# Kernel optimization log

Hardware: AMD Instinct MI355X
Metric: run time of the kernel (lower is better)

## Reference

```python
import jax, jax.numpy as jnp
import numpy as np

B, N, D = 8, 1024, 768
H = 12
HD = D // H


def setup_inputs() -> dict:
    key = jax.random.key(0)
    ks = jax.random.split(key, 9)
    s = 1.0 / np.sqrt(D)
    return {
        "x": jax.random.normal(ks[0], (B, N, D), dtype=jnp.float32),
        "Wq": jax.random.normal(ks[1], (D, D), dtype=jnp.float32) * s,
        "bq": jax.random.normal(ks[2], (D,), dtype=jnp.float32) * 0.02,
        "Wk": jax.random.normal(ks[3], (D, D), dtype=jnp.float32) * s,
        "bk": jax.random.normal(ks[4], (D,), dtype=jnp.float32) * 0.02,
        "Wv": jax.random.normal(ks[5], (D, D), dtype=jnp.float32) * s,
        "bv": jax.random.normal(ks[6], (D,), dtype=jnp.float32) * 0.02,
        "Wo": jax.random.normal(ks[7], (D, D), dtype=jnp.float32) * s,
        "bo": jax.random.normal(ks[8], (D,), dtype=jnp.float32) * 0.02,
    }


def _softmax_one(x):
    # quiet softmax: exp(x - max) / (1 + sum exp(x - max))
    x = x - jnp.max(x, axis=-1, keepdims=True)
    ex = jnp.exp(x)
    return ex / (1.0 + jnp.sum(ex, axis=-1, keepdims=True))


def reference(x, Wq, bq, Wk, bk, Wv, bv, Wo, bo):
    q = x @ Wq + bq  # [B,N,D]
    k = x @ Wk + bk
    v = x @ Wv + bv
    # split heads -> [B,H,N,HD]
    qs = q.reshape(B, N, H, HD).transpose(0, 2, 1, 3)
    ks = k.reshape(B, N, H, HD).transpose(0, 2, 1, 3)
    vs = v.reshape(B, N, H, HD).transpose(0, 2, 1, 3)
    scores = jnp.einsum("bhqd,bhkd->bhqk", qs, ks) / np.sqrt(HD)
    attn = _softmax_one(scores)  # quiet_attention=True
    ctx = jnp.einsum("bhqk,bhkd->bhqd", attn, vs)
    ctx = ctx.transpose(0, 2, 1, 3).reshape(B, N, D)
    return ctx @ Wo + bo
```

## Files before the change

### kernel.cpp

```cpp
#include <hip/hip_runtime.h>
#include <cstdint>

#define DEV __device__ __forceinline__

typedef __bf16 bf16x4 __attribute__((ext_vector_type(4)));
typedef __bf16 bf16x8 __attribute__((ext_vector_type(8)));
typedef float  floatx4 __attribute__((ext_vector_type(4)));
typedef float  floatx16 __attribute__((ext_vector_type(16)));
typedef unsigned uint4v __attribute__((ext_vector_type(4)));

constexpr int BB = 8, NSEQ = 1024, DMODEL = 768, NH = 12, HD = 64;
constexpr int MTOK = BB * NSEQ;
constexpr int NQKV = 3 * DMODEL;
constexpr float CS = 0.18033688011112042f;

DEV void async_copy16(void* lds, const void* g) {
    __builtin_amdgcn_global_load_lds(
        (__attribute__((address_space(1))) void*)(const_cast<void*>(g)),
        (__attribute__((address_space(3))) void*)lds,
        16, 0, 0);
}

DEV floatx4 mfma16x32(bf16x8 a, bf16x8 b, floatx4 c) {
    return __builtin_amdgcn_mfma_f32_16x16x32_bf16(a, b, c, 0, 0, 0);
}
DEV floatx16 mfma32x16(bf16x8 a, bf16x8 b, floatx16 c) {
    return __builtin_amdgcn_mfma_f32_32x32x16_bf16(a, b, c, 0, 0, 0);
}
DEV unsigned cvtpk(float a, float b) {
    unsigned r;
    asm("v_cvt_pk_bf16_f32 %0, %1, %2" : "=v"(r) : "v"(a), "v"(b));
    return r;
}
DEV void swap32(unsigned& x, unsigned& y) {
    asm("v_permlane32_swap_b32 %0, %1" : "+v"(x), "+v"(y));
}


__global__ __launch_bounds__(256) void k_prep(const float* __restrict__ x,
                                              __bf16* __restrict__ xb,
                                              const float* __restrict__ Wq,
                                              const float* __restrict__ Wk,
                                              const float* __restrict__ Wv,
                                              const float* __restrict__ Wo,
                                              __bf16* __restrict__ wtqkv,
                                              __bf16* __restrict__ wto,
                                              const float* __restrict__ bq,
                                              const float* __restrict__ bk,
                                              const float* __restrict__ bv,
                                              float* __restrict__ bqkv) {
    __shared__ float tile[32][33];
    int bid = blockIdx.x, t = threadIdx.x;
    if (bid < 6144) {
        int i = (bid * 256 + t) * 4;
        float4 v = *(const float4*)(x + i);
        bf16x4 o;
        o[0] = (__bf16)v.x; o[1] = (__bf16)v.y; o[2] = (__bf16)v.z; o[3] = (__bf16)v.w;
        *(bf16x4*)(xb + i) = o;
    } else if (bid < 8448) {
        int idx = bid - 6144;
        int z = idx / 576, rem = idx % 576;
        int k0 = (rem % 24) * 32, n0 = (rem / 24) * 32;
        const float* W = (z == 0) ? Wq : (z == 1) ? Wk : (z == 2) ? Wv : Wo;
        int tx = t & 31, ty = t >> 5;
#pragma unroll
        for (int p = 0; p < 4; p++)
            tile[ty + 8 * p][tx] = W[(size_t)(k0 + ty + 8 * p) * 768 + n0 + tx];
        __syncthreads();
        __bf16* out = (z < 3) ? (wtqkv + (size_t)z * 768 * 768) : wto;
#pragma unroll
        for (int p = 0; p < 4; p++)
            out[(size_t)(n0 + ty + 8 * p) * 768 + k0 + tx] = (__bf16)tile[tx][ty + 8 * p];
    } else {
        int i = (bid - 8448) * 256 + t;
        if (i < 768) bqkv[i] = bq[i];
        else if (i < 1536) bqkv[i] = bk[i - 768];
        else bqkv[i] = bv[i - 1536];
    }
}

__global__ __launch_bounds__(512) void k_qkv(const __bf16* __restrict__ A,
                                             const __bf16* __restrict__ Bt,
                                             const float* __restrict__ bias,
                                             __bf16* __restrict__ qfb,
                                             __bf16* __restrict__ kfb,
                                             __bf16* __restrict__ vfb) {
    constexpr int SLOT = 24576;
    __shared__ __align__(16) __bf16 lds[3 * SLOT];
    int t = threadIdx.x, lane = t & 63, w = t >> 6;
    int quad = lane >> 4, n16 = lane & 15;
    int wm = w >> 1, wn = w & 1;
    int m0 = blockIdx.x * 256, n0 = blockIdx.y * 128;
    floatx4 acc[4][4] = {};

    auto stage_part = [&](__bf16* slot, int k0, int p) {
        __bf16* As_ = slot;
        __bf16* Bs_ = slot + 16384;
#pragma unroll
        for (int i = 2 * p; i < 2 * p + 2; i++) {
            int off = t + i * 512;
            int row = off >> 3, pc = off & 7;
            int c = pc ^ (row & 7);
            async_copy16(&As_[row * 64 + pc * 8],
                         &A[(size_t)(m0 + row) * 768 + k0 + c * 8]);
        }
        {
            int off = t + p * 512;
            int row = off >> 3, pc = off & 7;
            int c = pc ^ (row & 7);
            async_copy16(&Bs_[row * 64 + pc * 8],
                         &Bt[(size_t)(n0 + row) * 768 + k0 + c * 8]);
        }
    };

    stage_part(lds, 0, 0);
    stage_part(lds, 0, 1);
    stage_part(lds + SLOT, 64, 0);
    stage_part(lds + SLOT, 64, 1);
    asm volatile("s_waitcnt vmcnt(6)\n\ts_barrier" ::: "memory");
    __builtin_amdgcn_sched_barrier(0);

#pragma unroll
    for (int kt = 0; kt < 12; kt++) {
        __bf16* As_ = lds + (kt % 3) * SLOT;
        __bf16* Bs_ = As_ + 16384;
        __bf16* pf = lds + ((kt + 2) % 3) * SLOT;
        int pk0 = (kt + 2) * 64;
        bool do_pf = (kt + 2 < 12);

#pragma unroll
        for (int kfi = 0; kfi < 2; kfi++) {
            if (do_pf) stage_part(pf, pk0, kfi);
            bf16x8 a[4], bfr[4];
#pragma unroll
            for (int rt = 0; rt < 4; rt++) {
                int row = wm * 64 + rt * 16 + n16;
                a[rt] = *(const bf16x8*)&As_[row * 64 + ((quad + 4 * kfi) ^ (row & 7)) * 8];
            }
#pragma unroll
            for (int ct = 0; ct < 4; ct++) {
                int row = wn * 64 + ct * 16 + n16;
                bfr[ct] = *(const bf16x8*)&Bs_[row * 64 + ((quad + 4 * kfi) ^ (row & 7)) * 8];
            }
            __builtin_amdgcn_s_setprio(1);
#pragma unroll
            for (int rt = 0; rt < 4; rt++)
#pragma unroll
                for (int ct = 0; ct < 4; ct++)
                    acc[rt][ct] = mfma16x32(a[rt], bfr[ct], acc[rt][ct]);
            __builtin_amdgcn_s_setprio(0);
        }

        if (kt < 11) {
            __builtin_amdgcn_sched_barrier(0);
            if (kt < 10) {
                asm volatile("s_waitcnt vmcnt(6)\n\ts_barrier" ::: "memory");
            } else {
                asm volatile("s_waitcnt vmcnt(0)\n\ts_barrier" ::: "memory");
            }
            __builtin_amdgcn_sched_barrier(0);
        }
    }

    if (n0 >= 1536) {
#pragma unroll
        for (int ct = 0; ct < 4; ct++) {
            int col = n0 + wn * 64 + ct * 16 + n16;
            float bs = bias[col];
            int cz = col - 1536;
            int hh = cz >> 6, hd = cz & 63;
            int mg = hd >> 5, l5v = hd & 31;
#pragma unroll
            for (int rt = 0; rt < 4; rt++) {
                int row0 = m0 + wm * 64 + rt * 16 + quad * 4;
                int bb = row0 >> 10, key = row0 & 1023;
                int iw = key >> 7, w_ = (key >> 5) & 3, kc = (key >> 4) & 1;
                int b5v = (key >> 3) & 1, j0 = key & 7;
                bf16x4 pk;
#pragma unroll
                for (int r = 0; r < 4; r++) pk[r] = (__bf16)(acc[rt][ct][r] + bs);
                size_t idx = (((((size_t)(bb * 12 + hh) * 8 + iw) * 4 + w_) * 2 + kc) * 2 + mg) * 512
                             + (size_t)(b5v * 32 + l5v) * 8 + j0;
                *(bf16x4*)&vfb[idx] = pk;
            }
        }
    } else {
        __bf16* dst = (n0 < 768) ? qfb : kfb;
        float mult = (n0 < 768) ? CS : 1.0f;
        bool isQ = (n0 < 768);
        int cofs = isQ ? 0 : 768;
#pragma unroll
        for (int ct = 0; ct < 4; ct++) {
            int col = n0 + wn * 64 + ct * 16 + n16;
            float bs = bias[col];
            int cz = col - cofs;
            int hh = cz >> 6, hd = cz & 63;
            int kfi = hd >> 4, b5v = (hd >> 3) & 1, j = hd & 7;
#pragma unroll
            for (int rt = 0; rt < 4; rt++) {
                int row0 = m0 + wm * 64 + rt * 16 + quad * 4;
                int bb = row0 >> 10, q10 = row0 & 1023;
                size_t idx;
                if (isQ) {
                    int qt = q10 >> 5, l5v = q10 & 31;
                    idx = (((size_t)(bb * 12 + hh) * 32 + qt) * 4 + kfi) * 512
                          + (size_t)(b5v * 32 + l5v) * 8 + j;
                } else {
                    int iw = q10 >> 7, w_ = (q10 >> 5) & 3, l5v = q10 & 31;
                    idx = ((((size_t)(bb * 12 + hh) * 8 + iw) * 4 + w_) * 4 + kfi) * 512
                          + (size_t)(b5v * 32 + l5v) * 8 + j;
                }
#pragma unroll
                for (int r = 0; r < 4; r++)
                    dst[idx + (size_t)r * 8] = (__bf16)((acc[rt][ct][r] + bs) * mult);
            }
        }
    }
}

template <typename OutT, int BN>
__global__ __launch_bounds__(256) void k_gemm(const __bf16* __restrict__ A,
                                              const __bf16* __restrict__ Bt,
                                              const float* __restrict__ bias,
                                              OutT* __restrict__ C, int Nn) {
    constexpr int CT = BN / 32;
    constexpr int NBI = BN / 32;
    __shared__ __align__(16) __bf16 As[128 * 64];
    __shared__ __align__(16) __bf16 Bs[BN * 64];
    int t = threadIdx.x, lane = t & 63, w = t >> 6;
    int quad = lane >> 4, n16 = lane & 15;
    int wm = w & 1, wn = w >> 1;
    int m0 = blockIdx.x * 128, n0 = blockIdx.y * BN;
    floatx4 acc[4][CT] = {};

    for (int k0 = 0; k0 < 768; k0 += 64) {
        __syncthreads();
#pragma unroll
        for (int i = 0; i < 4; i++) {
            int off = t + i * 256;
            int row = off >> 3, pc = off & 7;
            int c = pc ^ (row & 7);
            async_copy16(&As[row * 64 + pc * 8],
                         &A[(size_t)(m0 + row) * 768 + k0 + c * 8]);
        }
#pragma unroll
        for (int i = 0; i < NBI; i++) {
            int off = t + i * 256;
            int row = off >> 3, pc = off & 7;
            int c = pc ^ (row & 7);
            async_copy16(&Bs[row * 64 + pc * 8],
                         &Bt[(size_t)(n0 + row) * 768 + k0 + c * 8]);
        }
        __builtin_amdgcn_s_waitcnt(0);
        __syncthreads();
#pragma unroll
        for (int kfi = 0; kfi < 2; kfi++) {
            bf16x8 a[4], bfr[CT];
#pragma unroll
            for (int rt = 0; rt < 4; rt++) {
                int row = wm * 64 + rt * 16 + n16;
                a[rt] = *(const bf16x8*)&As[row * 64 + ((quad + 4 * kfi) ^ (row & 7)) * 8];
            }
#pragma unroll
            for (int ct = 0; ct < CT; ct++) {
                int row = wn * (BN / 2) + ct * 16 + n16;
                bfr[ct] = *(const bf16x8*)&Bs[row * 64 + ((quad + 4 * kfi) ^ (row & 7)) * 8];
            }
#pragma unroll
            for (int rt = 0; rt < 4; rt++)
#pragma unroll
                for (int ct = 0; ct < CT; ct++)
                    acc[rt][ct] = mfma16x32(a[rt], bfr[ct], acc[rt][ct]);
        }
    }

#pragma unroll
    for (int ct = 0; ct < CT; ct++) {
        int col = n0 + wn * (BN / 2) + ct * 16 + n16;
        float bs = bias[col];
#pragma unroll
        for (int rt = 0; rt < 4; rt++) {
#pragma unroll
            for (int r = 0; r < 4; r++) {
                int row = m0 + wm * 64 + rt * 16 + quad * 4 + r;
                C[(size_t)row * Nn + col] = (OutT)(acc[rt][ct][r] + bs);
            }
        }
    }
}

__global__ __launch_bounds__(256) void k_attn(const __bf16* __restrict__ QF,
                                              const __bf16* __restrict__ KF,
                                              const __bf16* __restrict__ VF,
                                              __bf16* __restrict__ ctx) {
    __shared__ __align__(16) unsigned char smem[18432];
    float* buf0 = (float*)smem;
    float* buf1 = (float*)(smem + 8704);
    float* Lsum = (float*)(smem + 17408);
    float* Pmax = (float*)(smem + 17920);

    int t = threadIdx.x, lane = t & 63, w = t >> 6;
    int l5 = lane & 31, b5 = lane >> 5;
    int id = blockIdx.x;
    int bB = id & 7;
    int seq = id >> 3;
    int h = seq % 12;
    int qt = seq / 12;
    int q0 = qt * 32;
    int bh = bB * NH + h;

    bf16x8 qf[4];
    {
        const __bf16* qp = QF + ((size_t)(bh * 32 + qt) * 4) * 512 + lane * 8;
#pragma unroll
        for (int kfi = 0; kfi < 4; kfi++)
            qf[kfi] = *(const bf16x8*)(qp + kfi * 512);
    }
    const __bf16* kp = KF + ((size_t)(bh * 8) * 4 + w) * 2048 + lane * 8;
    const __bf16* vp = VF + ((size_t)(bh * 8) * 4 + w) * 2048 + lane * 8;

    floatx16 acc[2] = {};
    float rs = 0.f, pm = 0.f;

    auto compute = [&](bf16x8 (&kf)[4], bf16x8 (&vf)[4]) {
        floatx16 s = {};
#pragma unroll
        for (int kfi = 0; kfi < 4; kfi++)
            s = mfma32x16(kf[kfi], qf[kfi], s);
        float p[16];
#pragma unroll
        for (int r = 0; r < 16; r++) {
            p[r] = __builtin_amdgcn_exp2f(s[r]);
            rs += p[r];
            pm = fmaxf(pm, p[r]);
        }
        unsigned x0 = cvtpk(p[0], p[1]),   y0 = cvtpk(p[4], p[5]);
        unsigned x1 = cvtpk(p[2], p[3]),   y1 = cvtpk(p[6], p[7]);
        unsigned x2 = cvtpk(p[8], p[9]),   y2 = cvtpk(p[12], p[13]);
        unsigned x3 = cvtpk(p[10], p[11]), y3 = cvtpk(p[14], p[15]);
        swap32(x0, y0); swap32(x1, y1); swap32(x2, y2); swap32(x3, y3);
        uint4v pa = {x0, x1, y0, y1};
        uint4v pbv = {x2, x3, y2, y3};
        bf16x8 P0 = __builtin_bit_cast(bf16x8, pa);
        bf16x8 P1 = __builtin_bit_cast(bf16x8, pbv);
        acc[0] = mfma32x16(vf[0], P0, acc[0]);
        acc[1] = mfma32x16(vf[1], P0, acc[1]);
        acc[0] = mfma32x16(vf[2], P1, acc[0]);
        acc[1] = mfma32x16(vf[3], P1, acc[1]);
    };

    bf16x8 ka[4], kb[4], vv[4];
#pragma unroll
    for (int f = 0; f < 4; f++) ka[f] = *(const bf16x8*)(kp + f * 512);
    kp += 8192;

    for (int i = 0; i < 8; i += 2) {
#pragma unroll
        for (int f = 0; f < 4; f++) kb[f] = *(const bf16x8*)(kp + f * 512);
        kp += 8192;
#pragma unroll
        for (int f = 0; f < 4; f++) vv[f] = *(const bf16x8*)(vp + f * 512);
        vp += 8192;
        compute(ka, vv);
        if (i < 6) {
#pragma unroll
            for (int f = 0; f < 4; f++) ka[f] = *(const bf16x8*)(kp + f * 512);
            kp += 8192;
        }
#pragma unroll
        for (int f = 0; f < 4; f++) vv[f] = *(const bf16x8*)(vp + f * 512);
        vp += 8192;
        compute(kb, vv);
    }

    rs += __shfl_xor(rs, 32);
    pm = fmaxf(pm, __shfl_xor(pm, 32));
    if (lane < 32) {
        Lsum[w * 32 + lane] = rs;
        Pmax[w * 32 + lane] = pm;
    }

    float* mybuf = (w & 1) ? buf1 : buf0;
    if (w < 2) {
#pragma unroll
        for (int mg = 0; mg < 2; mg++)
#pragma unroll
            for (int rq = 0; rq < 4; rq++) {
                floatx4 v = {acc[mg][rq * 4 + 0], acc[mg][rq * 4 + 1],
                             acc[mg][rq * 4 + 2], acc[mg][rq * 4 + 3]};
                *(floatx4*)&mybuf[l5 * 68 + mg * 32 + b5 * 4 + rq * 8] = v;
            }
    }
    __syncthreads();
    if (w >= 2) {
#pragma unroll
        for (int mg = 0; mg < 2; mg++)
#pragma unroll
            for (int rq = 0; rq < 4; rq++) {
                float* p = &mybuf[l5 * 68 + mg * 32 + b5 * 4 + rq * 8];
                floatx4 cur = *(const floatx4*)p;
                floatx4 v = {acc[mg][rq * 4 + 0], acc[mg][rq * 4 + 1],
                             acc[mg][rq * 4 + 2], acc[mg][rq * 4 + 3]};
                *(floatx4*)p = cur + v;
            }
    }
    __syncthreads();

    int qrow = t >> 3;
    int hh = (t & 7) * 8;
    float l = Lsum[qrow] + Lsum[32 + qrow] + Lsum[64 + qrow] + Lsum[96 + qrow];
    float pmx = fmaxf(fmaxf(Pmax[qrow], Pmax[32 + qrow]),
                      fmaxf(Pmax[64 + qrow], Pmax[96 + qrow]));
    float invd = 1.f / (pmx + l);
    floatx4 v0 = *(const floatx4*)&buf0[qrow * 68 + hh];
    floatx4 v1 = *(const floatx4*)&buf0[qrow * 68 + hh + 4];
    floatx4 u0 = *(const floatx4*)&buf1[qrow * 68 + hh];
    floatx4 u1 = *(const floatx4*)&buf1[qrow * 68 + hh + 4];
    bf16x8 o;
#pragma unroll
    for (int j = 0; j < 4; j++) o[j] = (__bf16)((v0[j] + u0[j]) * invd);
#pragma unroll
    for (int j = 0; j < 4; j++) o[j + 4] = (__bf16)((v1[j] + u1[j]) * invd);
    __bf16* dst = ctx + (size_t)(bB * NSEQ + q0 + qrow) * DMODEL + h * 64 + hh;
    *(bf16x8*)dst = o;
}

extern "C" void kernel_launch(void* const* d_in, const int* in_sizes, int n_in,
                              void* d_out, int out_size, void* d_ws, size_t ws_size,
                              hipStream_t stream) {
    (void)in_sizes; (void)n_in; (void)out_size;
    const float* x  = (const float*)d_in[0];
    const float* Wq = (const float*)d_in[1];
    const float* bq = (const float*)d_in[2];
    const float* Wk = (const float*)d_in[3];
    const float* bk = (const float*)d_in[4];
    const float* Wv = (const float*)d_in[5];
    const float* bv = (const float*)d_in[6];
    const float* Wo = (const float*)d_in[7];
    const float* bo = (const float*)d_in[8];
    float* out = (float*)d_out;

    char* ws = (char*)d_ws;
    size_t off = 0;
    auto alloc = [&](size_t bytes) {
        void* p = ws + off;
        off += (bytes + 255) & ~(size_t)255;
        return p;
    };
    __bf16* xb    = (__bf16*)alloc((size_t)MTOK * DMODEL * 2);
    __bf16* wtqkv = (__bf16*)alloc((size_t)NQKV * DMODEL * 2);
    __bf16* wto   = (__bf16*)alloc((size_t)DMODEL * DMODEL * 2);
    float*  bqkv  = (float*)alloc((size_t)NQKV * 4);
    __bf16* qfb   = (__bf16*)alloc((size_t)MTOK * DMODEL * 2);
    __bf16* kfb   = (__bf16*)alloc((size_t)MTOK * DMODEL * 2);
    __bf16* vfb   = (__bf16*)alloc((size_t)MTOK * DMODEL * 2);
    if (off > ws_size) return;
    __bf16* ctx = xb;

    k_prep<<<dim3(8457), dim3(256), 0, stream>>>(x, xb, Wq, Wk, Wv, Wo, wtqkv, wto,
                                                 bq, bk, bv, bqkv);
    k_qkv<<<dim3(32, 18), dim3(512), 0, stream>>>(xb, wtqkv, bqkv, qfb, kfb, vfb);
    k_attn<<<dim3(3072), dim3(256), 0, stream>>>(qfb, kfb, vfb, ctx);
    k_gemm<float, 64><<<dim3(64, 12), dim3(256), 0, stream>>>(
        ctx, wto, bo, out, DMODEL);
}
```

Before: 182.5 us.

## Shrink QKV GEMM tiles to 128x128 with BK=32 and pipeline output projection

The QKV GEMM moves from 512-thread 256x128 blocks with K=64 stages to 256-thread 128x128 blocks with K=32 triple-buffered stages. This gives twice as many blocks and uses much less LDS per block, which should raise occupancy and improve load balance across CUs. The output projection GEMM, which used to load synchronously with a full waitcnt(0) every iteration, is rewritten with the same triple-buffered async-copy pipeline. The trade-off is more barriers per K step and lower operand reuse per block.

```diff
diff --git a/kernel.cpp b/kernel.cpp
--- a/kernel.cpp
+++ b/kernel.cpp
@@ -79,82 +79,75 @@
     }
 }
 
-__global__ __launch_bounds__(512) void k_qkv(const __bf16* __restrict__ A,
+__global__ __launch_bounds__(256) void k_qkv(const __bf16* __restrict__ A,
                                              const __bf16* __restrict__ Bt,
                                              const float* __restrict__ bias,
                                              __bf16* __restrict__ qfb,
                                              __bf16* __restrict__ kfb,
                                              __bf16* __restrict__ vfb) {
-    constexpr int SLOT = 24576;
+    constexpr int SLOT = 8192;
     __shared__ __align__(16) __bf16 lds[3 * SLOT];
     int t = threadIdx.x, lane = t & 63, w = t >> 6;
     int quad = lane >> 4, n16 = lane & 15;
-    int wm = w >> 1, wn = w & 1;
-    int m0 = blockIdx.x * 256, n0 = blockIdx.y * 128;
+    int wm = w & 1, wn = w >> 1;
+    int m0 = blockIdx.x * 128, n0 = blockIdx.y * 128;
     floatx4 acc[4][4] = {};
 
-    auto stage_part = [&](__bf16* slot, int k0, int p) {
+    auto stage_tile = [&](__bf16* slot, int k0) {
         __bf16* As_ = slot;
-        __bf16* Bs_ = slot + 16384;
-#pragma unroll
-        for (int i = 2 * p; i < 2 * p + 2; i++) {
-            int off = t + i * 512;
-            int row = off >> 3, pc = off & 7;
-            int c = pc ^ (row & 7);
-            async_copy16(&As_[row * 64 + pc * 8],
+        __bf16* Bs_ = slot + 4096;
+#pragma unroll
+        for (int i = 0; i < 2; i++) {
+            int off = t + i * 256;
+            int row = off >> 2, pc = off & 3;
+            int c = pc ^ ((row >> 1) & 3);
+            async_copy16(&As_[row * 32 + pc * 8],
                          &A[(size_t)(m0 + row) * 768 + k0 + c * 8]);
         }
-        {
-            int off = t + p * 512;
-            int row = off >> 3, pc = off & 7;
-            int c = pc ^ (row & 7);
-            async_copy16(&Bs_[row * 64 + pc * 8],
+#pragma unroll
+        for (int i = 0; i < 2; i++) {
+            int off = t + i * 256;
+            int row = off >> 2, pc = off & 3;
+            int c = pc ^ ((row >> 1) & 3);
+            async_copy16(&Bs_[row * 32 + pc * 8],
                          &Bt[(size_t)(n0 + row) * 768 + k0 + c * 8]);
         }
     };
 
-    stage_part(lds, 0, 0);
-    stage_part(lds, 0, 1);
-    stage_part(lds + SLOT, 64, 0);
-    stage_part(lds + SLOT, 64, 1);
-    asm volatile("s_waitcnt vmcnt(6)\n\ts_barrier" ::: "memory");
+    stage_tile(lds, 0);
+    stage_tile(lds + SLOT, 32);
+    asm volatile("s_waitcnt vmcnt(4)\n\ts_barrier" ::: "memory");
     __builtin_amdgcn_sched_barrier(0);
 
 #pragma unroll
-    for (int kt = 0; kt < 12; kt++) {
+    for (int kt = 0; kt < 24; kt++) {
         __bf16* As_ = lds + (kt % 3) * SLOT;
-        __bf16* Bs_ = As_ + 16384;
-        __bf16* pf = lds + ((kt + 2) % 3) * SLOT;
-        int pk0 = (kt + 2) * 64;
-        bool do_pf = (kt + 2 < 12);
-
-#pragma unroll
-        for (int kfi = 0; kfi < 2; kfi++) {
-            if (do_pf) stage_part(pf, pk0, kfi);
-            bf16x8 a[4], bfr[4];
-#pragma unroll
-            for (int rt = 0; rt < 4; rt++) {
-                int row = wm * 64 + rt * 16 + n16;
-                a[rt] = *(const bf16x8*)&As_[row * 64 + ((quad + 4 * kfi) ^ (row & 7)) * 8];
-            }
-#pragma unroll
-            for (int ct = 0; ct < 4; ct++) {
-                int row = wn * 64 + ct * 16 + n16;
-                bfr[ct] = *(const bf16x8*)&Bs_[row * 64 + ((quad + 4 * kfi) ^ (row & 7)) * 8];
-            }
-            __builtin_amdgcn_s_setprio(1);
-#pragma unroll
-            for (int rt = 0; rt < 4; rt++)
-#pragma unroll
-                for (int ct = 0; ct < 4; ct++)
-                    acc[rt][ct] = mfma16x32(a[rt], bfr[ct], acc[rt][ct]);
-            __builtin_amdgcn_s_setprio(0);
-        }
-
-        if (kt < 11) {
+        __bf16* Bs_ = As_ + 4096;
+        if (kt + 2 < 24) stage_tile(lds + ((kt + 2) % 3) * SLOT, (kt + 2) * 32);
+
+        bf16x8 a[4], bfr[4];
+#pragma unroll
+        for (int rt = 0; rt < 4; rt++) {
+            int row = wm * 64 + rt * 16 + n16;
+            a[rt] = *(const bf16x8*)&As_[row * 32 + (quad ^ ((row >> 1) & 3)) * 8];
+        }
+#pragma unroll
+        for (int ct = 0; ct < 4; ct++) {
+            int row = wn * 64 + ct * 16 + n16;
+            bfr[ct] = *(const bf16x8*)&Bs_[row * 32 + (quad ^ ((row >> 1) & 3)) * 8];
+        }
+        __builtin_amdgcn_s_setprio(1);
+#pragma unroll
+        for (int rt = 0; rt < 4; rt++)
+#pragma unroll
+            for (int ct = 0; ct < 4; ct++)
+                acc[rt][ct] = mfma16x32(a[rt], bfr[ct], acc[rt][ct]);
+        __builtin_amdgcn_s_setprio(0);
+
+        if (kt < 23) {
             __builtin_amdgcn_sched_barrier(0);
-            if (kt < 10) {
-                asm volatile("s_waitcnt vmcnt(6)\n\ts_barrier" ::: "memory");
+            if (kt < 22) {
+                asm volatile("s_waitcnt vmcnt(4)\n\ts_barrier" ::: "memory");
             } else {
                 asm volatile("s_waitcnt vmcnt(0)\n\ts_barrier" ::: "memory");
             }
@@ -218,72 +211,89 @@
     }
 }
 
-template <typename OutT, int BN>
-__global__ __launch_bounds__(256) void k_gemm(const __bf16* __restrict__ A,
-                                              const __bf16* __restrict__ Bt,
-                                              const float* __restrict__ bias,
-                                              OutT* __restrict__ C, int Nn) {
-    constexpr int CT = BN / 32;
-    constexpr int NBI = BN / 32;
-    __shared__ __align__(16) __bf16 As[128 * 64];
-    __shared__ __align__(16) __bf16 Bs[BN * 64];
+__global__ __launch_bounds__(256) void k_oproj(const __bf16* __restrict__ A,
+                                               const __bf16* __restrict__ Bt,
+                                               const float* __restrict__ bias,
+                                               float* __restrict__ C) {
+    constexpr int SLOT = 6144;
+    __shared__ __align__(16) __bf16 lds[3 * SLOT];
     int t = threadIdx.x, lane = t & 63, w = t >> 6;
     int quad = lane >> 4, n16 = lane & 15;
     int wm = w & 1, wn = w >> 1;
-    int m0 = blockIdx.x * 128, n0 = blockIdx.y * BN;
-    floatx4 acc[4][CT] = {};
-
-    for (int k0 = 0; k0 < 768; k0 += 64) {
-        __syncthreads();
-#pragma unroll
-        for (int i = 0; i < 4; i++) {
+    int m0 = blockIdx.x * 128, n0 = blockIdx.y * 64;
+    floatx4 acc[4][2] = {};
+
+    auto stage_tile = [&](__bf16* slot, int k0) {
+        __bf16* As_ = slot;
+        __bf16* Bs_ = slot + 4096;
+#pragma unroll
+        for (int i = 0; i < 2; i++) {
             int off = t + i * 256;
-            int row = off >> 3, pc = off & 7;
-            int c = pc ^ (row & 7);
-            async_copy16(&As[row * 64 + pc * 8],
+            int row = off >> 2, pc = off & 3;
+            int c = pc ^ ((row >> 1) & 3);
+            async_copy16(&As_[row * 32 + pc * 8],
                          &A[(size_t)(m0 + row) * 768 + k0 + c * 8]);
         }
-#pragma unroll
-        for (int i = 0; i < NBI; i++) {
-            int off = t + i * 256;
-            int row = off >> 3, pc = off & 7;
-            int c = pc ^ (row & 7);
-            async_copy16(&Bs[row * 64 + pc * 8],
+        {
+            int off = t;
+            int row = off >> 2, pc = off & 3;
+            int c = pc ^ ((row >> 1) & 3);
+            async_copy16(&Bs_[row * 32 + pc * 8],
                          &Bt[(size_t)(n0 + row) * 768 + k0 + c * 8]);
         }
-        __builtin_amdgcn_s_waitcnt(0);
-        __syncthreads();
-#pragma unroll
-        for (int kfi = 0; kfi < 2; kfi++) {
-            bf16x8 a[4], bfr[CT];
-#pragma unroll
-            for (int rt = 0; rt < 4; rt++) {
-                int row = wm * 64 + rt * 16 + n16;
-                a[rt] = *(const bf16x8*)&As[row * 64 + ((quad + 4 * kfi) ^ (row & 7)) * 8];
-            }
-#pragma unroll
-            for (int ct = 0; ct < CT; ct++) {
-                int row = wn * (BN / 2) + ct * 16 + n16;
-                bfr[ct] = *(const bf16x8*)&Bs[row * 64 + ((quad + 4 * kfi) ^ (row & 7)) * 8];
-            }
-#pragma unroll
-            for (int rt = 0; rt < 4; rt++)
-#pragma unroll
-                for (int ct = 0; ct < CT; ct++)
-                    acc[rt][ct] = mfma16x32(a[rt], bfr[ct], acc[rt][ct]);
-        }
-    }
-
-#pragma unroll
-    for (int ct = 0; ct < CT; ct++) {
-        int col = n0 + wn * (BN / 2) + ct * 16 + n16;
+    };
+
+    stage_tile(lds, 0);
+    stage_tile(lds + SLOT, 32);
+    asm volatile("s_waitcnt vmcnt(3)\n\ts_barrier" ::: "memory");
+    __builtin_amdgcn_sched_barrier(0);
+
+#pragma unroll
+    for (int kt = 0; kt < 24; kt++) {
+        __bf16* As_ = lds + (kt % 3) * SLOT;
+        __bf16* Bs_ = As_ + 4096;
+        if (kt + 2 < 24) stage_tile(lds + ((kt + 2) % 3) * SLOT, (kt + 2) * 32);
+
+        bf16x8 a[4], bfr[2];
+#pragma unroll
+        for (int rt = 0; rt < 4; rt++) {
+            int row = wm * 64 + rt * 16 + n16;
+            a[rt] = *(const bf16x8*)&As_[row * 32 + (quad ^ ((row >> 1) & 3)) * 8];
+        }
+#pragma unroll
+        for (int ct = 0; ct < 2; ct++) {
+            int row = wn * 32 + ct * 16 + n16;
+            bfr[ct] = *(const bf16x8*)&Bs_[row * 32 + (quad ^ ((row >> 1) & 3)) * 8];
+        }
+        __builtin_amdgcn_s_setprio(1);
+#pragma unroll
+        for (int rt = 0; rt < 4; rt++)
+#pragma unroll
+            for (int ct = 0; ct < 2; ct++)
+                acc[rt][ct] = mfma16x32(a[rt], bfr[ct], acc[rt][ct]);
+        __builtin_amdgcn_s_setprio(0);
+
+        if (kt < 23) {
+            __builtin_amdgcn_sched_barrier(0);
+            if (kt < 22) {
+                asm volatile("s_waitcnt vmcnt(3)\n\ts_barrier" ::: "memory");
+            } else {
+                asm volatile("s_waitcnt vmcnt(0)\n\ts_barrier" ::: "memory");
+            }
+            __builtin_amdgcn_sched_barrier(0);
+        }
+    }
+
+#pragma unroll
+    for (int ct = 0; ct < 2; ct++) {
+        int col = n0 + wn * 32 + ct * 16 + n16;
         float bs = bias[col];
 #pragma unroll
         for (int rt = 0; rt < 4; rt++) {
 #pragma unroll
             for (int r = 0; r < 4; r++) {
                 int row = m0 + wm * 64 + rt * 16 + quad * 4 + r;
-                C[(size_t)row * Nn + col] = (OutT)(acc[rt][ct][r] + bs);
+                C[(size_t)row * DMODEL + col] = acc[rt][ct][r] + bs;
             }
         }
     }
@@ -459,8 +469,7 @@
 
     k_prep<<<dim3(8457), dim3(256), 0, stream>>>(x, xb, Wq, Wk, Wv, Wo, wtqkv, wto,
                                                  bq, bk, bv, bqkv);
-    k_qkv<<<dim3(32, 18), dim3(512), 0, stream>>>(xb, wtqkv, bqkv, qfb, kfb, vfb);
+    k_qkv<<<dim3(64, 18), dim3(256), 0, stream>>>(xb, wtqkv, bqkv, qfb, kfb, vfb);
     k_attn<<<dim3(3072), dim3(256), 0, stream>>>(qfb, kfb, vfb, ctx);
-    k_gemm<float, 64><<<dim3(64, 12), dim3(256), 0, stream>>>(
-        ctx, wto, bo, out, DMODEL);
-}
+    k_oproj<<<dim3(64, 12), dim3(256), 0, stream>>>(ctx, wto, bo, out);
+}
```

Result: slower. 189.5 us (+3.8%).
